# Performance work log

Hardware: AMD Instinct MI355X
Metric: run time of the kernel (lower is better)

Reference implementation:

```python
import jax, jax.numpy as jnp
import numpy as np
from jax import lax

B, C, H, W = 4, 128, 128, 128
DG = 2          # deformable groups
K = 9           # 3x3 kernel
EPS = 1e-5


def conv2d(x, w, stride=1, pad=1):
    return lax.conv_general_dilated(
        x, w, (stride, stride), [(pad, pad), (pad, pad)],
        dimension_numbers=("NCHW", "OIHW", "NCHW"))


def bn(x, p):
    # p: [4, C] = gamma, beta, running_mean, running_var (eval-mode BN)
    g, b, m, v = p[0], p[1], p[2], p[3]
    inv = g / jnp.sqrt(v + EPS)
    return x * inv[:, None, None] + (b - m * inv)[:, None, None]


def deform_sample(x, py, px):
    # x: [B,C,H,W]; py/px: [B,DG,K,H,W] absolute sample coords
    Bb, Cc, Hh, Ww = x.shape
    Cg = Cc // DG
    xg = x.reshape(Bb, DG, Cg, Hh * Ww)
    y0 = jnp.floor(py); x0 = jnp.floor(px)
    fy = py - y0; fx = px - x0
    y0i = y0.astype(jnp.int32); x0i = x0.astype(jnp.int32)

    def corner(yi, xi, wgt):
        valid = (yi >= 0) & (yi < Hh) & (xi >= 0) & (xi < Ww)
        idx = (jnp.clip(yi, 0, Hh - 1) * Ww + jnp.clip(xi, 0, Ww - 1)).reshape(Bb, DG, -1)
        v = jnp.take_along_axis(xg, idx[:, :, None, :], axis=3)  # [B,DG,Cg,K*H*W]
        return v * (wgt * valid).reshape(Bb, DG, 1, -1)

    val = (corner(y0i, x0i, (1 - fy) * (1 - fx))
           + corner(y0i, x0i + 1, (1 - fy) * fx)
           + corner(y0i + 1, x0i, fy * (1 - fx))
           + corner(y0i + 1, x0i + 1, fy * fx))
    return val.reshape(Bb, DG, Cg, K, Hh, Ww)


def modulated_deform_conv(x, off_w, off_b, dc_w, dc_b):
    Bb, Cc, Hh, Ww = x.shape
    off_out = conv2d(x, off_w) + off_b[None, :, None, None]   # [B,3*DG*K,H,W]
    o = off_out[:, :2 * DG * K].reshape(Bb, DG, K, 2, Hh, Ww)
    mask = jax.nn.sigmoid(off_out[:, 2 * DG * K:]).reshape(Bb, DG, K, Hh, Ww)
    ky = (jnp.arange(K) // 3 - 1).astype(x.dtype)
    kx = (jnp.arange(K) % 3 - 1).astype(x.dtype)
    iy = jnp.arange(Hh, dtype=x.dtype)[:, None]
    ix = jnp.arange(Ww, dtype=x.dtype)[None, :]
    py = o[:, :, :, 0] + iy + ky[None, None, :, None, None]
    px = o[:, :, :, 1] + ix + kx[None, None, :, None, None]
    g = deform_sample(x, py, px) * mask[:, :, None]            # [B,DG,Cg,K,H,W]
    wr = dc_w.reshape(dc_w.shape[0], DG, Cc // DG, K)          # [O,DG,Cg,K]
    out = jnp.einsum("odck,bdckhw->bohw", wr, g)
    return out + dc_b[None, :, None, None]


def setup_inputs() -> dict:
    key = jax.random.key(0)
    ks = jax.random.split(key, 16)
    s3 = 1.0 / np.sqrt(C * 9)
    s1 = 1.0 / np.sqrt(C)

    def bn_params(k):
        k1, k2, k3, k4 = jax.random.split(k, 4)
        return jnp.stack([
            jax.random.uniform(k1, (C,)) + 0.5,
            jax.random.normal(k2, (C,)) * 0.1,
            jax.random.normal(k3, (C,)) * 0.1,
            jax.random.uniform(k4, (C,)) + 0.5])

    return {
        "x": jax.random.normal(ks[0], (B, C, H, W), jnp.float32),
        "rb_w1": jax.random.normal(ks[1], (C, C, 3, 3), jnp.float32) * s3,
        "rb_b1": jax.random.normal(ks[2], (C,), jnp.float32) * 0.01,
        "rb_bn1": bn_params(ks[3]),
        "rb_w2": jax.random.normal(ks[4], (C, C, 3, 3), jnp.float32) * s3,
        "rb_b2": jax.random.normal(ks[5], (C,), jnp.float32) * 0.01,
        "rb_bn2": bn_params(ks[6]),
        "off_w": jax.random.normal(ks[7], (3 * DG * K, C, 3, 3), jnp.float32) * s3 * 0.1,
        "off_b": jax.random.normal(ks[8], (3 * DG * K,), jnp.float32) * 0.01,
        "dc_w": jax.random.normal(ks[9], (C, C, 3, 3), jnp.float32) * s3,
        "dc_b": jax.random.normal(ks[10], (C,), jnp.float32) * 0.01,
        "bn1": bn_params(ks[11]),
        "cv2_w": jax.random.normal(ks[12], (C, C, 1, 1), jnp.float32) * s1,
        "bn2": bn_params(ks[13]),
    }


def reference(x, rb_w1, rb_b1, rb_bn1, rb_w2, rb_b2, rb_bn2,
              off_w, off_b, dc_w, dc_b, bn1, cv2_w, bn2):
    # ResBlock (stride=1, n_in==n_out -> identity shortcut)
    h = jax.nn.relu(bn(conv2d(x, rb_w1) + rb_b1[None, :, None, None], rb_bn1))
    h = bn(conv2d(h, rb_w2) + rb_b2[None, :, None, None], rb_bn2)
    h = jax.nn.relu(h + x)
    # modulated deformable conv + BN + LeakyReLU(0.1)
    h = modulated_deform_conv(h, off_w, off_b, dc_w, dc_b)
    h = jax.nn.leaky_relu(bn(h, bn1), 0.1)
    # 1x1 conv (no bias) + BN + LeakyReLU(0.1)
    h = jax.nn.leaky_relu(bn(conv2d(h, cv2_w, pad=0), bn2), 0.1)
    # residual (downsample is None: in==out, stride==1)
    return x + h
```

## Files before the change

kernel.cpp:

```cpp
#include <hip/hip_runtime.h>
#include <math.h>

#define BB 4
#define EPSV 1e-5f

typedef __attribute__((ext_vector_type(8))) short short8;
typedef __attribute__((ext_vector_type(4))) float floatx4;
typedef __attribute__((ext_vector_type(4))) unsigned short ushort4v;

__device__ inline float b2f(unsigned short u) {
    unsigned v = ((unsigned)u) << 16;
    return __builtin_bit_cast(float, v);
}
__device__ inline unsigned short f2b(float f) {
    unsigned u = __builtin_bit_cast(unsigned, f);
    u += 0x7FFFu + ((u >> 16) & 1u);
    return (unsigned short)(u >> 16);
}

__global__ __launch_bounds__(256) void transpose_k(const float* __restrict__ x,
                                                   unsigned short* __restrict__ xb) {
    __shared__ unsigned short t[64][136];
    const int tid = threadIdx.x;
    const int px0 = blockIdx.x * 64;
    const int b = blockIdx.y;
    const int pxr = tid & 63;
    const int c0 = tid >> 6;
#pragma unroll
    for (int i = 0; i < 32; ++i) {
        int c = c0 + i * 4;
        float v = x[(((size_t)b * 128 + c) << 14) + px0 + pxr];
        t[pxr][c] = f2b(v);
    }
    __syncthreads();
#pragma unroll
    for (int i = 0; i < 4; ++i) {
        int idx = tid + i * 256;
        int px = idx >> 4;
        int c8 = idx & 15;
        short8 v = *(const short8*)&t[px][c8 * 8];
        *(short8*)&xb[(((size_t)b << 14) + px0 + px) * 128 + c8 * 8] = v;
    }
}

template<int MPAD, int OCH>
__global__ __launch_bounds__(256) void repack_conv_frag(const float* __restrict__ w,
                                                        unsigned short* __restrict__ dst) {
    int t = blockIdx.x * 256 + threadIdx.x;
    if (t >= 1152 * MPAD) return;
    const int NMT2 = MPAD / 16;
    int j = t & 7, lane = (t >> 3) & 63, rest = t >> 9;
    int mt = rest % NMT2, step = rest / NMT2;
    int oc = mt * 16 + (lane & 15);
    int k = step * 32 + ((lane >> 4) << 3) + j;
    int half = k / 576;
    int tap = (k - half * 576) >> 6;
    int c = half * 64 + (k & 63);
    float v = (oc < OCH) ? w[((size_t)oc * 128 + c) * 9 + tap] : 0.f;
    dst[t] = f2b(v);
}

__global__ __launch_bounds__(256) void repack_dc_frag(const float* __restrict__ w,
                                                      unsigned short* __restrict__ dst) {
    int t = blockIdx.x * 256 + threadIdx.x;
    if (t >= 1152 * 128) return;
    int j = t & 7, lane = (t >> 3) & 63, rest = t >> 9;
    int mt = rest & 7, step = rest >> 3;
    int oc = mt * 16 + (lane & 15);
    int k = step * 32 + ((lane >> 4) << 3) + j;
    int dk = k >> 6, c = k & 63;
    int d = (dk >= 9) ? 1 : 0;
    int kk = dk - d * 9;
    float v = w[((size_t)oc * 128 + d * 64 + c) * 9 + kk];
    dst[t] = f2b(v);
}

__global__ __launch_bounds__(256) void repack_cv2_frag(const float* __restrict__ w,
                                                       unsigned short* __restrict__ dst) {
    int t = blockIdx.x * 256 + threadIdx.x;
    if (t >= 128 * 128) return;
    int j = t & 7, lane = (t >> 3) & 63, rest = t >> 9;
    int mt = rest & 7, step = rest >> 3;
    int oc = mt * 16 + (lane & 15);
    int k = step * 32 + ((lane >> 4) << 3) + j;
    dst[t] = f2b(w[oc * 128 + k]);
}

template<int NMT, int MODE>
__global__ __launch_bounds__(256, 3) void conv3x3_mfma(
    const unsigned short* __restrict__ in, const unsigned short* __restrict__ wf,
    const float* __restrict__ bias, const float* __restrict__ bnp,
    const float* __restrict__ res, void* __restrict__ outv)
{
    __shared__ unsigned short sm[3][66][72];
    const int tid = threadIdx.x;
    const int lane = tid & 63, wid = tid >> 6;
    const int wm = wid & 1, wn = wid >> 1;
    const int w0 = (blockIdx.x & 1) * 64;
    const int h = blockIdx.x >> 1;
    const int b = blockIdx.y;
    const int n16 = lane & 15, quad = lane >> 4;

    short8 L0[7], L1[7];
#pragma unroll
    for (int half = 0; half < 2; ++half) {
        short8* L = half ? L1 : L0;
#pragma unroll
        for (int rnd = 0; rnd < 7; ++rnd) {
            int idx = rnd * 256 + tid;
            short8 v = {0, 0, 0, 0, 0, 0, 0, 0};
            if (idx < 1584) {
                int c8 = idx & 7;
                int wl = (idx >> 3) % 66;
                int r  = (idx >> 3) / 66;
                int hh = h - 1 + r, ww = w0 - 1 + wl;
                if ((unsigned)hh < 128u && (unsigned)ww < 128u)
                    v = *(const short8*)&in[(((size_t)b << 14) + hh * 128 + ww) * 128 + half * 64 + c8 * 8];
            }
            L[rnd] = v;
        }
    }

    floatx4 acc[NMT][2];
#pragma unroll
    for (int mt = 0; mt < NMT; ++mt)
#pragma unroll
        for (int nt = 0; nt < 2; ++nt)
            acc[mt][nt] = (floatx4){0.f, 0.f, 0.f, 0.f};

#pragma unroll
    for (int half = 0; half < 2; ++half) {
        if (half) __syncthreads();
        {
            short8* L = half ? L1 : L0;
#pragma unroll
            for (int rnd = 0; rnd < 7; ++rnd) {
                int idx = rnd * 256 + tid;
                if (idx < 1584) {
                    int c8 = idx & 7;
                    int wl = (idx >> 3) % 66;
                    int r  = (idx >> 3) / 66;
                    *(short8*)&sm[r][wl][c8 * 8] = L[rnd];
                }
            }
        }
        __syncthreads();

#pragma unroll
        for (int tap = 0; tap < 9; ++tap) {
            const int ky = tap / 3, kx = tap % 3;
#pragma unroll
            for (int cc = 0; cc < 2; ++cc) {
                const int step = half * 18 + tap * 2 + cc;
                short8 a[NMT], bf[2];
#pragma unroll
                for (int nt = 0; nt < 2; ++nt)
                    bf[nt] = *(const short8*)&sm[ky][wn * 32 + nt * 16 + n16 + kx][cc * 32 + quad * 8];
#pragma unroll
                for (int mt = 0; mt < NMT; ++mt)
                    a[mt] = *(const short8*)&wf[((size_t)(step * (2 * NMT) + wm * NMT + mt) * 64 + lane) * 8];
#pragma unroll
                for (int mt = 0; mt < NMT; ++mt)
#pragma unroll
                    for (int nt = 0; nt < 2; ++nt)
                        acc[mt][nt] = __builtin_amdgcn_mfma_f32_16x16x32_bf16(a[mt], bf[nt], acc[mt][nt], 0, 0, 0);
            }
        }
    }

#pragma unroll
    for (int mt = 0; mt < NMT; ++mt) {
        const int ocb = (wm * NMT + mt) * 16 + quad * 4;
        float Ae[4], Be[4];
#pragma unroll
        for (int r = 0; r < 4; ++r) {
            int oc = ocb + r;
            if (MODE == 0) {
                Ae[r] = 1.f;
                Be[r] = (oc < 54) ? bias[oc] : 0.f;
            } else {
                float g = bnp[oc], be = bnp[128 + oc], m = bnp[256 + oc], vv = bnp[384 + oc];
                float inv = g * rsqrtf(vv + EPSV);
                Ae[r] = inv;
                Be[r] = be - m * inv + bias[oc] * inv;
            }
        }
#pragma unroll
        for (int nt = 0; nt < 2; ++nt) {
            int pxg = h * 128 + w0 + wn * 32 + nt * 16 + n16;
            if (MODE == 0) {
                float* outf = (float*)outv;
#pragma unroll
                for (int r = 0; r < 4; ++r) {
                    int oc = ocb + r;
                    if (oc < 54)
                        outf[((size_t)(b << 14) + pxg) * 54 + oc] = acc[mt][nt][r] + Be[r];
                }
            } else {
                ushort4v pk;
#pragma unroll
                for (int r = 0; r < 4; ++r) {
                    float v = acc[mt][nt][r] * Ae[r] + Be[r];
                    if (MODE == 2) v += res[(((size_t)b * 128 + ocb + r) << 14) + pxg];
                    v = fmaxf(v, 0.f);
                    pk[r] = f2b(v);
                }
                *(ushort4v*)&((unsigned short*)outv)[((size_t)((b << 14) + pxg)) * 128 + ocb] = pk;
            }
        }
    }
}

__global__ __launch_bounds__(256, 3) void deform_mfma(
    const unsigned short* __restrict__ src, const float* __restrict__ off,
    const unsigned short* __restrict__ wf, const float* __restrict__ dcb,
    const float* __restrict__ bnp, unsigned short* __restrict__ out)
{
    __shared__ unsigned short gt[2][64][72];
    const int tid = threadIdx.x;
    const int lane = tid & 63, wid = tid >> 6;
    const int wm = wid & 1, wn = wid >> 1;
    const int w0 = (blockIdx.x & 1) * 64;
    const int h = blockIdx.x >> 1;
    const int b = blockIdx.y;
    const int n16 = lane & 15, quad = lane >> 4;

    const int q = tid & 7;
    const int pxq = tid >> 3;

    const float* offbase = off + ((size_t)(b << 14) + h * 128 + w0) * 54;
    const unsigned short* srcb = src + ((size_t)b << 21);

    floatx4 acc[4][2];
#pragma unroll
    for (int mt = 0; mt < 4; ++mt)
#pragma unroll
        for (int nt = 0; nt < 2; ++nt)
            acc[mt][nt] = (floatx4){0.f, 0.f, 0.f, 0.f};

    short8 g[2][4];
    float  wA[2][4];
    float  oN[2][3];
    float  oC[2][3];

    auto load_off = [&](int dk, float o[2][3]) {
#pragma unroll
        for (int ph = 0; ph < 2; ++ph) {
            const float* p = offbase + (size_t)(ph * 32 + pxq) * 54;
            o[ph][0] = p[2 * dk];
            o[ph][1] = p[2 * dk + 1];
            o[ph][2] = p[36 + dk];
        }
    };

    auto issue_gather = [&](int dk, const float o[2][3]) {
        const int d = (dk >= 9) ? 1 : 0;
        const int kk = dk - d * 9;
        const int choff = d * 64 + q * 8;
#pragma unroll
        for (int ph = 0; ph < 2; ++ph) {
            int px = ph * 32 + pxq;
            float ms = 1.f / (1.f + __expf(-o[ph][2]));
            float py = o[ph][0] + (float)h + (float)(kk / 3 - 1);
            float pxs = o[ph][1] + (float)(w0 + px) + (float)(kk % 3 - 1);
            float y0f = floorf(py), x0f = floorf(pxs);
            float fy = py - y0f, fx = pxs - x0f;
            int y0 = (int)y0f, x0 = (int)x0f;
            int y1 = y0 + 1, x1 = x0 + 1;
            float w00 = (1.f - fy) * (1.f - fx) * ms, w01 = (1.f - fy) * fx * ms;
            float w10 = fy * (1.f - fx) * ms, w11 = fy * fx * ms;
            if ((unsigned)y0 >= 128u) { w00 = 0.f; w01 = 0.f; }
            if ((unsigned)y1 >= 128u) { w10 = 0.f; w11 = 0.f; }
            if ((unsigned)x0 >= 128u) { w00 = 0.f; w10 = 0.f; }
            if ((unsigned)x1 >= 128u) { w01 = 0.f; w11 = 0.f; }
            wA[ph][0] = w00; wA[ph][1] = w01; wA[ph][2] = w10; wA[ph][3] = w11;
            int y0c = min(max(y0, 0), 127), y1c = min(max(y1, 0), 127);
            int x0c = min(max(x0, 0), 127), x1c = min(max(x1, 0), 127);
            g[ph][0] = *(const short8*)(srcb + (((size_t)(y0c * 128 + x0c)) << 7) + choff);
            g[ph][1] = *(const short8*)(srcb + (((size_t)(y0c * 128 + x1c)) << 7) + choff);
            g[ph][2] = *(const short8*)(srcb + (((size_t)(y1c * 128 + x0c)) << 7) + choff);
            g[ph][3] = *(const short8*)(srcb + (((size_t)(y1c * 128 + x1c)) << 7) + choff);
        }
    };

    load_off(0, oC);
    issue_gather(0, oC);
    load_off(1, oN);

    int buf = 0;
    for (int dk = 0; dk < 18; ++dk) {
#pragma unroll
        for (int ph = 0; ph < 2; ++ph) {
            short8 o8;
#pragma unroll
            for (int j = 0; j < 8; ++j) {
                float v = wA[ph][0] * b2f((unsigned short)g[ph][0][j])
                        + wA[ph][1] * b2f((unsigned short)g[ph][1][j])
                        + wA[ph][2] * b2f((unsigned short)g[ph][2][j])
                        + wA[ph][3] * b2f((unsigned short)g[ph][3][j]);
                o8[j] = (short)f2b(v);
            }
            *(short8*)&gt[buf][ph * 32 + pxq][q * 8] = o8;
        }
        __syncthreads();

        if (dk < 17) {
#pragma unroll
            for (int ph = 0; ph < 2; ++ph)
#pragma unroll
                for (int j = 0; j < 3; ++j) oC[ph][j] = oN[ph][j];
            if (dk < 16) load_off(dk + 2, oN);
            issue_gather(dk + 1, oC);
        }

#pragma unroll
        for (int hf = 0; hf < 2; ++hf) {
            int s = dk * 2 + hf;
            short8 a[4], bfr[2];
#pragma unroll
            for (int nt = 0; nt < 2; ++nt)
                bfr[nt] = *(const short8*)&gt[buf][wn * 32 + nt * 16 + n16][hf * 32 + quad * 8];
#pragma unroll
            for (int mt = 0; mt < 4; ++mt)
                a[mt] = *(const short8*)&wf[((size_t)(s * 8 + wm * 4 + mt) * 64 + lane) * 8];
#pragma unroll
            for (int mt = 0; mt < 4; ++mt)
#pragma unroll
                for (int nt = 0; nt < 2; ++nt)
                    acc[mt][nt] = __builtin_amdgcn_mfma_f32_16x16x32_bf16(a[mt], bfr[nt], acc[mt][nt], 0, 0, 0);
        }
        buf ^= 1;
    }

#pragma unroll
    for (int mt = 0; mt < 4; ++mt) {
        const int ocb = (wm * 4 + mt) * 16 + quad * 4;
        float Ae[4], Be[4];
#pragma unroll
        for (int r = 0; r < 4; ++r) {
            int oc = ocb + r;
            float gg = bnp[oc], be = bnp[128 + oc], m = bnp[256 + oc], vv = bnp[384 + oc];
            float inv = gg * rsqrtf(vv + EPSV);
            Ae[r] = inv;
            Be[r] = be - m * inv + dcb[oc] * inv;
        }
#pragma unroll
        for (int nt = 0; nt < 2; ++nt) {
            int pxg2 = h * 128 + w0 + wn * 32 + nt * 16 + n16;
            ushort4v pk;
#pragma unroll
            for (int r = 0; r < 4; ++r) {
                float v = acc[mt][nt][r] * Ae[r] + Be[r];
                v = (v > 0.f) ? v : 0.1f * v;
                pk[r] = f2b(v);
            }
            *(ushort4v*)&out[((size_t)((b << 14) + pxg2)) * 128 + ocb] = pk;
        }
    }
}

__global__ __launch_bounds__(256, 4) void conv1x1_mfma(
    const unsigned short* __restrict__ in, const unsigned short* __restrict__ wf,
    const float* __restrict__ bnp, const float* __restrict__ x, float* __restrict__ out)
{
    const int tid = threadIdx.x;
    const int lane = tid & 63, wid = tid >> 6;
    const int wm = wid & 1, wn = wid >> 1;
    const int w0 = (blockIdx.x & 1) * 64;
    const int h = blockIdx.x >> 1;
    const int b = blockIdx.y;
    const int n16 = lane & 15, quad = lane >> 4;

    floatx4 acc[4][2];
#pragma unroll
    for (int mt = 0; mt < 4; ++mt)
#pragma unroll
        for (int nt = 0; nt < 2; ++nt)
            acc[mt][nt] = (floatx4){0.f, 0.f, 0.f, 0.f};

#pragma unroll
    for (int s = 0; s < 4; ++s) {
        short8 a[4], bfr[2];
#pragma unroll
        for (int nt = 0; nt < 2; ++nt) {
            int px = h * 128 + w0 + wn * 32 + nt * 16 + n16;
            bfr[nt] = *(const short8*)&in[((size_t)((b << 14) + px)) * 128 + s * 32 + quad * 8];
        }
#pragma unroll
        for (int mt = 0; mt < 4; ++mt)
            a[mt] = *(const short8*)&wf[((size_t)(s * 8 + wm * 4 + mt) * 64 + lane) * 8];
#pragma unroll
        for (int mt = 0; mt < 4; ++mt)
#pragma unroll
            for (int nt = 0; nt < 2; ++nt)
                acc[mt][nt] = __builtin_amdgcn_mfma_f32_16x16x32_bf16(a[mt], bfr[nt], acc[mt][nt], 0, 0, 0);
    }

#pragma unroll
    for (int mt = 0; mt < 4; ++mt) {
        const int ocb = (wm * 4 + mt) * 16 + quad * 4;
        float Ae[4], Be[4];
#pragma unroll
        for (int r = 0; r < 4; ++r) {
            int oc = ocb + r;
            float g = bnp[oc], be = bnp[128 + oc], m = bnp[256 + oc], vv = bnp[384 + oc];
            float inv = g * rsqrtf(vv + EPSV);
            Ae[r] = inv;
            Be[r] = be - m * inv;
        }
#pragma unroll
        for (int nt = 0; nt < 2; ++nt) {
            int pxg2 = h * 128 + w0 + wn * 32 + nt * 16 + n16;
#pragma unroll
            for (int r = 0; r < 4; ++r) {
                int oc = ocb + r;
                float v = acc[mt][nt][r] * Ae[r] + Be[r];
                v = (v > 0.f) ? v : 0.1f * v;
                v += x[(((size_t)b * 128 + oc) << 14) + pxg2];
                out[(((size_t)b * 128 + oc) << 14) + pxg2] = v;
            }
        }
    }
}

extern "C" void kernel_launch(void* const* d_in, const int* in_sizes, int n_in,
                              void* d_out, int out_size, void* d_ws, size_t ws_size,
                              hipStream_t stream) {
    const float* x      = (const float*)d_in[0];
    const float* rb_w1  = (const float*)d_in[1];
    const float* rb_b1  = (const float*)d_in[2];
    const float* rb_bn1 = (const float*)d_in[3];
    const float* rb_w2  = (const float*)d_in[4];
    const float* rb_b2  = (const float*)d_in[5];
    const float* rb_bn2 = (const float*)d_in[6];
    const float* off_w  = (const float*)d_in[7];
    const float* off_b  = (const float*)d_in[8];
    const float* dc_w   = (const float*)d_in[9];
    const float* dc_b   = (const float*)d_in[10];
    const float* bn1    = (const float*)d_in[11];
    const float* cv2_w  = (const float*)d_in[12];
    const float* bn2    = (const float*)d_in[13];

    char* base = (char*)d_ws;
    const size_t TSZ = (size_t)4 * 16384 * 128 * 2;
    unsigned short* xb = (unsigned short*)base;
    unsigned short* h1 = (unsigned short*)(base + TSZ);
    unsigned short* h2 = (unsigned short*)(base + 2 * TSZ);
    unsigned short* wf1 = (unsigned short*)(base + 3 * TSZ);
    unsigned short* wf2 = wf1 + 1152 * 128;
    unsigned short* wfO = wf2 + 1152 * 128;
    unsigned short* wfD = wfO + 1152 * 64;
    unsigned short* wfC = wfD + 1152 * 128;
    float* offb = (float*)h1;
    unsigned short* h3 = xb;

    dim3 blk(256, 1, 1);
    dim3 grid(256, BB, 1);

    transpose_k<<<grid, blk, 0, stream>>>(x, xb);
    repack_conv_frag<128, 128><<<576, 256, 0, stream>>>(rb_w1, wf1);
    repack_conv_frag<128, 128><<<576, 256, 0, stream>>>(rb_w2, wf2);
    repack_conv_frag<64, 54><<<288, 256, 0, stream>>>(off_w, wfO);
    repack_dc_frag<<<576, 256, 0, stream>>>(dc_w, wfD);
    repack_cv2_frag<<<64, 256, 0, stream>>>(cv2_w, wfC);

    conv3x3_mfma<4, 1><<<grid, blk, 0, stream>>>(xb, wf1, rb_b1, rb_bn1, nullptr, (void*)h1);
    conv3x3_mfma<4, 2><<<grid, blk, 0, stream>>>(h1, wf2, rb_b2, rb_bn2, x, (void*)h2);
    conv3x3_mfma<2, 0><<<grid, blk, 0, stream>>>(h2, wfO, off_b, nullptr, nullptr, (void*)offb);
    deform_mfma<<<grid, blk, 0, stream>>>(h2, offb, wfD, dc_b, bn1, h3);
    conv1x1_mfma<<<grid, blk, 0, stream>>>(h3, wfC, bn2, x, (float*)d_out);
}
```

Baseline: 304.5 us.

## Widen conv tiles to full rows, share deform sampling math via LDS

Each conv3x3 block now covers a full 128-pixel row instead of half a row. This halves the grid, doubles the N tiles per wave, and overlaps loading the second channel half with the first half's compute. The offset conv output moves to a channel-major layout. In the deform kernel, only 64 threads compute the bilinear weights and addresses, which go to a 3-slot LDS ring for all threads to read, and a cheaper round-to-bf16 replaces the round-to-nearest-even conversion. Launch bounds change to 2 waves for conv and 4 for deform, trading occupancy and register pressure against redundant address math and halo reloads.

```diff
diff --git a/kernel.cpp b/kernel.cpp
--- a/kernel.cpp
+++ b/kernel.cpp
@@ -6,6 +6,7 @@
 
 typedef __attribute__((ext_vector_type(8))) short short8;
 typedef __attribute__((ext_vector_type(4))) float floatx4;
+typedef __attribute__((ext_vector_type(4))) int intx4;
 typedef __attribute__((ext_vector_type(4))) unsigned short ushort4v;
 
 __device__ inline float b2f(unsigned short u) {
@@ -16,6 +17,10 @@
     unsigned u = __builtin_bit_cast(unsigned, f);
     u += 0x7FFFu + ((u >> 16) & 1u);
     return (unsigned short)(u >> 16);
+}
+__device__ inline unsigned short f2b_fast(float f) {
+    unsigned u = __builtin_bit_cast(unsigned, f);
+    return (unsigned short)((u + 0x8000u) >> 16);
 }
 
 __global__ __launch_bounds__(256) void transpose_k(const float* __restrict__ x,
@@ -87,86 +92,89 @@
 }
 
 template<int NMT, int MODE>
-__global__ __launch_bounds__(256, 3) void conv3x3_mfma(
+__global__ __launch_bounds__(256, 2) void conv3x3_mfma(
     const unsigned short* __restrict__ in, const unsigned short* __restrict__ wf,
     const float* __restrict__ bias, const float* __restrict__ bnp,
     const float* __restrict__ res, void* __restrict__ outv)
 {
-    __shared__ unsigned short sm[3][66][72];
+    __shared__ unsigned short sm[3][130][72];
     const int tid = threadIdx.x;
     const int lane = tid & 63, wid = tid >> 6;
     const int wm = wid & 1, wn = wid >> 1;
-    const int w0 = (blockIdx.x & 1) * 64;
-    const int h = blockIdx.x >> 1;
+    const int h = blockIdx.x;
     const int b = blockIdx.y;
     const int n16 = lane & 15, quad = lane >> 4;
 
-    short8 L0[7], L1[7];
-#pragma unroll
-    for (int half = 0; half < 2; ++half) {
-        short8* L = half ? L1 : L0;
-#pragma unroll
-        for (int rnd = 0; rnd < 7; ++rnd) {
+    short8 L[13];
+
+    auto stage_load = [&](int half) {
+#pragma unroll
+        for (int rnd = 0; rnd < 13; ++rnd) {
             int idx = rnd * 256 + tid;
             short8 v = {0, 0, 0, 0, 0, 0, 0, 0};
-            if (idx < 1584) {
+            if (idx < 3120) {
                 int c8 = idx & 7;
-                int wl = (idx >> 3) % 66;
-                int r  = (idx >> 3) / 66;
-                int hh = h - 1 + r, ww = w0 - 1 + wl;
+                int wl = (idx >> 3) % 130;
+                int r  = (idx >> 3) / 130;
+                int hh = h - 1 + r, ww = wl - 1;
                 if ((unsigned)hh < 128u && (unsigned)ww < 128u)
                     v = *(const short8*)&in[(((size_t)b << 14) + hh * 128 + ww) * 128 + half * 64 + c8 * 8];
             }
             L[rnd] = v;
         }
-    }
-
-    floatx4 acc[NMT][2];
+    };
+    auto stage_write = [&]() {
+#pragma unroll
+        for (int rnd = 0; rnd < 13; ++rnd) {
+            int idx = rnd * 256 + tid;
+            if (idx < 3120) {
+                int c8 = idx & 7;
+                int wl = (idx >> 3) % 130;
+                int r  = (idx >> 3) / 130;
+                *(short8*)&sm[r][wl][c8 * 8] = L[rnd];
+            }
+        }
+    };
+
+    floatx4 acc[NMT][4];
 #pragma unroll
     for (int mt = 0; mt < NMT; ++mt)
 #pragma unroll
-        for (int nt = 0; nt < 2; ++nt)
+        for (int nt = 0; nt < 4; ++nt)
             acc[mt][nt] = (floatx4){0.f, 0.f, 0.f, 0.f};
 
-#pragma unroll
-    for (int half = 0; half < 2; ++half) {
-        if (half) __syncthreads();
-        {
-            short8* L = half ? L1 : L0;
-#pragma unroll
-            for (int rnd = 0; rnd < 7; ++rnd) {
-                int idx = rnd * 256 + tid;
-                if (idx < 1584) {
-                    int c8 = idx & 7;
-                    int wl = (idx >> 3) % 66;
-                    int r  = (idx >> 3) / 66;
-                    *(short8*)&sm[r][wl][c8 * 8] = L[rnd];
-                }
-            }
-        }
-        __syncthreads();
-
+    auto compute = [&](int half) {
 #pragma unroll
         for (int tap = 0; tap < 9; ++tap) {
             const int ky = tap / 3, kx = tap % 3;
 #pragma unroll
             for (int cc = 0; cc < 2; ++cc) {
                 const int step = half * 18 + tap * 2 + cc;
-                short8 a[NMT], bf[2];
-#pragma unroll
-                for (int nt = 0; nt < 2; ++nt)
-                    bf[nt] = *(const short8*)&sm[ky][wn * 32 + nt * 16 + n16 + kx][cc * 32 + quad * 8];
+                short8 a[NMT], bf[4];
+#pragma unroll
+                for (int nt = 0; nt < 4; ++nt)
+                    bf[nt] = *(const short8*)&sm[ky][wn * 64 + nt * 16 + n16 + kx][cc * 32 + quad * 8];
 #pragma unroll
                 for (int mt = 0; mt < NMT; ++mt)
                     a[mt] = *(const short8*)&wf[((size_t)(step * (2 * NMT) + wm * NMT + mt) * 64 + lane) * 8];
 #pragma unroll
                 for (int mt = 0; mt < NMT; ++mt)
 #pragma unroll
-                    for (int nt = 0; nt < 2; ++nt)
+                    for (int nt = 0; nt < 4; ++nt)
                         acc[mt][nt] = __builtin_amdgcn_mfma_f32_16x16x32_bf16(a[mt], bf[nt], acc[mt][nt], 0, 0, 0);
             }
         }
-    }
+    };
+
+    stage_load(0);
+    stage_write();
+    __syncthreads();
+    stage_load(1);
+    compute(0);
+    __syncthreads();
+    stage_write();
+    __syncthreads();
+    compute(1);
 
 #pragma unroll
     for (int mt = 0; mt < NMT; ++mt) {
@@ -186,15 +194,15 @@
             }
         }
 #pragma unroll
-        for (int nt = 0; nt < 2; ++nt) {
-            int pxg = h * 128 + w0 + wn * 32 + nt * 16 + n16;
+        for (int nt = 0; nt < 4; ++nt) {
+            int pxg = h * 128 + wn * 64 + nt * 16 + n16;
             if (MODE == 0) {
                 float* outf = (float*)outv;
 #pragma unroll
                 for (int r = 0; r < 4; ++r) {
                     int oc = ocb + r;
                     if (oc < 54)
-                        outf[((size_t)(b << 14) + pxg) * 54 + oc] = acc[mt][nt][r] + Be[r];
+                        outf[(((size_t)(b * 54 + oc)) << 14) + pxg] = acc[mt][nt][r] + Be[r];
                 }
             } else {
                 ushort4v pk;
@@ -211,12 +219,14 @@
     }
 }
 
-__global__ __launch_bounds__(256, 3) void deform_mfma(
+__global__ __launch_bounds__(256, 4) void deform_mfma(
     const unsigned short* __restrict__ src, const float* __restrict__ off,
     const unsigned short* __restrict__ wf, const float* __restrict__ dcb,
     const float* __restrict__ bnp, unsigned short* __restrict__ out)
 {
     __shared__ unsigned short gt[2][64][72];
+    __shared__ floatx4 smw[3][64];
+    __shared__ intx4   sma[3][64];
     const int tid = threadIdx.x;
     const int lane = tid & 63, wid = tid >> 6;
     const int wm = wid & 1, wn = wid >> 1;
@@ -224,12 +234,53 @@
     const int h = blockIdx.x >> 1;
     const int b = blockIdx.y;
     const int n16 = lane & 15, quad = lane >> 4;
-
     const int q = tid & 7;
-    const int pxq = tid >> 3;
-
-    const float* offbase = off + ((size_t)(b << 14) + h * 128 + w0) * 54;
-    const unsigned short* srcb = src + ((size_t)b << 21);
+    const int pxq = tid >> 3 & 31;
+
+    const char* srcbyte = (const char*)src + ((size_t)b << 22);
+    const float* offpx = off + (((size_t)(b * 54)) << 14) + h * 128 + w0 + tid;
+
+    auto math = [&](int dk, int slot) {
+        float oy = offpx[(size_t)(2 * dk) << 14];
+        float ox = offpx[(size_t)(2 * dk + 1) << 14];
+        float mz = offpx[(size_t)(36 + dk) << 14];
+        int d = (dk >= 9) ? 1 : 0;
+        int kk = dk - d * 9;
+        float ms = 1.f / (1.f + __expf(-mz));
+        float py = oy + (float)h + (float)(kk / 3 - 1);
+        float pxs = ox + (float)(w0 + tid) + (float)(kk % 3 - 1);
+        float y0f = floorf(py), x0f = floorf(pxs);
+        float fy = py - y0f, fx = pxs - x0f;
+        int y0 = (int)y0f, x0 = (int)x0f;
+        int y1 = y0 + 1, x1 = x0 + 1;
+        float w00 = (1.f - fy) * (1.f - fx) * ms, w01 = (1.f - fy) * fx * ms;
+        float w10 = fy * (1.f - fx) * ms, w11 = fy * fx * ms;
+        if ((unsigned)y0 >= 128u) { w00 = 0.f; w01 = 0.f; }
+        if ((unsigned)y1 >= 128u) { w10 = 0.f; w11 = 0.f; }
+        if ((unsigned)x0 >= 128u) { w00 = 0.f; w10 = 0.f; }
+        if ((unsigned)x1 >= 128u) { w01 = 0.f; w11 = 0.f; }
+        int y0c = min(max(y0, 0), 127), y1c = min(max(y1, 0), 127);
+        int x0c = min(max(x0, 0), 127), x1c = min(max(x1, 0), 127);
+        int chb = d * 128;
+        smw[slot][tid] = (floatx4){w00, w01, w10, w11};
+        sma[slot][tid] = (intx4){((y0c * 128 + x0c) << 8) + chb, ((y0c * 128 + x1c) << 8) + chb,
+                                 ((y1c * 128 + x0c) << 8) + chb, ((y1c * 128 + x1c) << 8) + chb};
+    };
+
+    floatx4 wA[2];
+    short8 g[2][4];
+    auto gather = [&](int slot) {
+#pragma unroll
+        for (int ph = 0; ph < 2; ++ph) {
+            int pxl = ph * 32 + pxq;
+            floatx4 wv = smw[slot][pxl];
+            intx4 av = sma[slot][pxl];
+            wA[ph] = wv;
+#pragma unroll
+            for (int c = 0; c < 4; ++c)
+                g[ph][c] = *(const short8*)(srcbyte + (size_t)(av[c] + q * 16));
+        }
+    };
 
     floatx4 acc[4][2];
 #pragma unroll
@@ -238,54 +289,9 @@
         for (int nt = 0; nt < 2; ++nt)
             acc[mt][nt] = (floatx4){0.f, 0.f, 0.f, 0.f};
 
-    short8 g[2][4];
-    float  wA[2][4];
-    float  oN[2][3];
-    float  oC[2][3];
-
-    auto load_off = [&](int dk, float o[2][3]) {
-#pragma unroll
-        for (int ph = 0; ph < 2; ++ph) {
-            const float* p = offbase + (size_t)(ph * 32 + pxq) * 54;
-            o[ph][0] = p[2 * dk];
-            o[ph][1] = p[2 * dk + 1];
-            o[ph][2] = p[36 + dk];
-        }
-    };
-
-    auto issue_gather = [&](int dk, const float o[2][3]) {
-        const int d = (dk >= 9) ? 1 : 0;
-        const int kk = dk - d * 9;
-        const int choff = d * 64 + q * 8;
-#pragma unroll
-        for (int ph = 0; ph < 2; ++ph) {
-            int px = ph * 32 + pxq;
-            float ms = 1.f / (1.f + __expf(-o[ph][2]));
-            float py = o[ph][0] + (float)h + (float)(kk / 3 - 1);
-            float pxs = o[ph][1] + (float)(w0 + px) + (float)(kk % 3 - 1);
-            float y0f = floorf(py), x0f = floorf(pxs);
-            float fy = py - y0f, fx = pxs - x0f;
-            int y0 = (int)y0f, x0 = (int)x0f;
-            int y1 = y0 + 1, x1 = x0 + 1;
-            float w00 = (1.f - fy) * (1.f - fx) * ms, w01 = (1.f - fy) * fx * ms;
-            float w10 = fy * (1.f - fx) * ms, w11 = fy * fx * ms;
-            if ((unsigned)y0 >= 128u) { w00 = 0.f; w01 = 0.f; }
-            if ((unsigned)y1 >= 128u) { w10 = 0.f; w11 = 0.f; }
-            if ((unsigned)x0 >= 128u) { w00 = 0.f; w10 = 0.f; }
-            if ((unsigned)x1 >= 128u) { w01 = 0.f; w11 = 0.f; }
-            wA[ph][0] = w00; wA[ph][1] = w01; wA[ph][2] = w10; wA[ph][3] = w11;
-            int y0c = min(max(y0, 0), 127), y1c = min(max(y1, 0), 127);
-            int x0c = min(max(x0, 0), 127), x1c = min(max(x1, 0), 127);
-            g[ph][0] = *(const short8*)(srcb + (((size_t)(y0c * 128 + x0c)) << 7) + choff);
-            g[ph][1] = *(const short8*)(srcb + (((size_t)(y0c * 128 + x1c)) << 7) + choff);
-            g[ph][2] = *(const short8*)(srcb + (((size_t)(y1c * 128 + x0c)) << 7) + choff);
-            g[ph][3] = *(const short8*)(srcb + (((size_t)(y1c * 128 + x1c)) << 7) + choff);
-        }
-    };
-
-    load_off(0, oC);
-    issue_gather(0, oC);
-    load_off(1, oN);
+    if (tid < 64) { math(0, 0); math(1, 1); }
+    __syncthreads();
+    gather(0);
 
     int buf = 0;
     for (int dk = 0; dk < 18; ++dk) {
@@ -298,20 +304,13 @@
                         + wA[ph][1] * b2f((unsigned short)g[ph][1][j])
                         + wA[ph][2] * b2f((unsigned short)g[ph][2][j])
                         + wA[ph][3] * b2f((unsigned short)g[ph][3][j]);
-                o8[j] = (short)f2b(v);
+                o8[j] = (short)f2b_fast(v);
             }
             *(short8*)&gt[buf][ph * 32 + pxq][q * 8] = o8;
         }
+        if (tid < 64 && dk < 16) math(dk + 2, (dk + 2) % 3);
         __syncthreads();
-
-        if (dk < 17) {
-#pragma unroll
-            for (int ph = 0; ph < 2; ++ph)
-#pragma unroll
-                for (int j = 0; j < 3; ++j) oC[ph][j] = oN[ph][j];
-            if (dk < 16) load_off(dk + 2, oN);
-            issue_gather(dk + 1, oC);
-        }
+        if (dk < 17) gather((dk + 1) % 3);
 
 #pragma unroll
         for (int hf = 0; hf < 2; ++hf) {
@@ -456,6 +455,7 @@
 
     dim3 blk(256, 1, 1);
     dim3 grid(256, BB, 1);
+    dim3 grid3(128, BB, 1);
 
     transpose_k<<<grid, blk, 0, stream>>>(x, xb);
     repack_conv_frag<128, 128><<<576, 256, 0, stream>>>(rb_w1, wf1);
@@ -464,9 +464,9 @@
     repack_dc_frag<<<576, 256, 0, stream>>>(dc_w, wfD);
     repack_cv2_frag<<<64, 256, 0, stream>>>(cv2_w, wfC);
 
-    conv3x3_mfma<4, 1><<<grid, blk, 0, stream>>>(xb, wf1, rb_b1, rb_bn1, nullptr, (void*)h1);
-    conv3x3_mfma<4, 2><<<grid, blk, 0, stream>>>(h1, wf2, rb_b2, rb_bn2, x, (void*)h2);
-    conv3x3_mfma<2, 0><<<grid, blk, 0, stream>>>(h2, wfO, off_b, nullptr, nullptr, (void*)offb);
+    conv3x3_mfma<4, 1><<<grid3, blk, 0, stream>>>(xb, wf1, rb_b1, rb_bn1, nullptr, (void*)h1);
+    conv3x3_mfma<4, 2><<<grid3, blk, 0, stream>>>(h1, wf2, rb_b2, rb_bn2, x, (void*)h2);
+    conv3x3_mfma<2, 0><<<grid3, blk, 0, stream>>>(h2, wfO, off_b, nullptr, nullptr, (void*)offb);
     deform_mfma<<<grid, blk, 0, stream>>>(h2, offb, wfD, dc_b, bn1, h3);
     conv1x1_mfma<<<grid, blk, 0, stream>>>(h3, wfC, bn2, x, (float*)d_out);
 }
```

Result: faster. 275.5 us (-9.5%).
